# Kernel optimization log

Measured on AMD Instinct MI355X. Metric: run time of the kernel, lower is better.

The kernel has to match this reference:

```python
import jax, jax.numpy as jnp
import numpy as np

N_PTS = 65536      # query points (ray samples)
N_NODES = 4096     # deformation-graph nodes
K = 20             # neighbors, hardcoded in the module
D_PE = 32          # positional-encoding channels (sliced off, unused)
DIS_THRESH = 0.00021
FAR_VAL = 1e9


def setup_inputs() -> dict:
    key = jax.random.key(0)
    k1, k2, k3, k4, k5 = jax.random.split(key, 5)
    inputs = jax.random.normal(k1, (N_PTS, 3 + D_PE), dtype=jnp.float32)
    vd = jax.random.normal(k2, (N_NODES, 3), dtype=jnp.float32)
    R = jax.random.normal(k3, (N_NODES, 3, 3), dtype=jnp.float32)
    g = jax.random.normal(k4, (N_NODES, 3), dtype=jnp.float32)
    t = jax.random.normal(k5, (N_NODES, 3), dtype=jnp.float32) * 0.1
    return {"inputs": inputs, "vd": vd, "R": R, "g": g, "t": t}


def reference(inputs, vd, R, g, t):
    pts = inputs[:, :3]  # [N,3]; inputs[:,3:] (positional encoding) is unused

    # --- KNN (knn_points semantics: squared L2 dists, ascending) ---
    d2 = (jnp.sum(pts * pts, axis=-1, keepdims=True)
          + jnp.sum(vd * vd, axis=-1)[None, :]
          - 2.0 * pts @ vd.T)                      # [N, n]
    neg_d, idx = jax.lax.top_k(-d2, K)             # smallest d2 first
    dis = -neg_d                                   # [N,K] squared dists, ascending

    # --- neighbor weights: w = (1 - d/d_max)^2, normalized ---
    dis_max = jnp.max(dis, axis=-1, keepdims=True)
    w = jnp.square(1.0 - dis / dis_max)
    w = w / jnp.sum(w, axis=-1, keepdims=True)     # [N,K] (K=20 > 1, so no ones override)

    # --- per-neighbor gather + rigid transform: p = R^T (x - g - t) + g ---
    Rg = R[idx]                                    # [N,K,3,3]
    gg = g[idx]                                    # [N,K,3]
    tg = t[idx]                                    # [N,K,3]
    x = pts[:, None, :] - gg - tg                  # [N,K,3]
    p = jnp.einsum('nkji,nkj->nki', Rg, x) + gg    # R^T @ x, [N,K,3]
    R_inv = jnp.swapaxes(Rg, -1, -2)               # [N,K,3,3]

    # --- weighted blend over K neighbors ---
    p_blend = jnp.sum(p * w[:, :, None], axis=1)               # [N,3]
    R_blend = jnp.sum(R_inv * w[:, :, None, None], axis=1)     # [N,3,3]

    # --- far-point masking on x-coordinate ---
    far = dis[:, 0] > DIS_THRESH
    p_blend = p_blend.at[:, 0].set(jnp.where(far, FAR_VAL, p_blend[:, 0]))
    return p_blend, R_blend
```

## Files before the change

### kernel.cpp

```cpp
#include <hip/hip_runtime.h>
#include <stdint.h>


#define NPTS   65536
#define NNODES 4096
#define KSEL   20
#define CAP    32
#define BT     256
#define AFRAG_BYTES  (NNODES * 64)
#define WS_NEEDED    AFRAG_BYTES

typedef __attribute__((ext_vector_type(8)))  short short8;
typedef __attribute__((ext_vector_type(16))) float f32x16;

__device__ __forceinline__ uint32_t umin32(uint32_t a, uint32_t b) { return a < b ? a : b; }
__device__ __forceinline__ uint32_t umax32(uint32_t a, uint32_t b) { return a > b ? a : b; }
__device__ __forceinline__ void cmpswap(uint32_t& a, uint32_t& b) {
  const uint32_t lo = umin32(a, b), hi = umax32(a, b); a = lo; b = hi;
}
__device__ __forceinline__ void insert20(uint32_t m[KSEL], uint32_t x) {
#pragma unroll
  for (int k = KSEL - 1; k >= 1; --k)
    m[k] = umin32(m[k], umax32(m[k - 1], x));
  m[0] = umin32(m[0], x);
}
__device__ __forceinline__ float thr_from(uint32_t m19) {
  return __uint_as_float(umin32((m19 >> 12) << 11, 0x7F7FFFFFu));
}
__device__ __forceinline__ unsigned short f2bf(float x) {
  uint32_t u = __float_as_uint(x);
  return (unsigned short)((u + 0x7FFFu + ((u >> 16) & 1u)) >> 16);
}
__device__ __forceinline__ float bf2f(unsigned short h) {
  return __uint_as_float(((uint32_t)h) << 16);
}

__global__ void dg_prep(const float* __restrict__ vd,
                        unsigned short* __restrict__ aF) {
  const int j = blockIdx.x * 256 + threadIdx.x;
  const float v0 = vd[j * 3 + 0], v1 = vd[j * 3 + 1], v2 = vd[j * 3 + 2];
  unsigned short H[3], M[3], L[3];
  const float vc[3] = {v0, v1, v2};
#pragma unroll
  for (int c = 0; c < 3; ++c) {
    H[c] = f2bf(vc[c]);
    const float r1 = vc[c] - bf2f(H[c]);
    M[c] = f2bf(r1);
    const float r2 = r1 - bf2f(M[c]);
    L[c] = f2bf(r2);
  }
  const float sv = v0 * v0 + v1 * v1 + v2 * v2;
  const unsigned short svH = f2bf(sv);
  const float rs1 = sv - bf2f(svH);
  const unsigned short svM = f2bf(rs1);
  const unsigned short svL = f2bf(rs1 - bf2f(svM));

  unsigned short* o = aF + j * 32;
  o[0]=H[0]; o[1]=H[1]; o[2]=H[2]; o[3]=M[0]; o[4]=M[1]; o[5]=M[2];
  o[6]=L[0]; o[7]=L[1]; o[8]=L[2]; o[9]=H[0]; o[10]=H[1]; o[11]=H[2];
  o[12]=M[0]; o[13]=M[1]; o[14]=M[2]; o[15]=L[0];
  o[16]=L[1]; o[17]=L[2]; o[18]=H[0]; o[19]=H[1]; o[20]=H[2];
  o[21]=M[0]; o[22]=M[1]; o[23]=M[2];
  o[24]=L[0]; o[25]=L[1]; o[26]=L[2];
  o[27]=(unsigned short)svH; o[28]=(unsigned short)svM; o[29]=(unsigned short)svL;
  o[30]=0x3F80; o[31]=0x3F80;
}

__global__ __launch_bounds__(BT, 4) void dg_mfma(
    const float* __restrict__ inp, const float* __restrict__ vd,
    const float* __restrict__ Rm, const float* __restrict__ gv,
    const float* __restrict__ tv, const short8* __restrict__ aF,
    float* __restrict__ out)
{
  __shared__ uint32_t st[CAP * BT];
  const int tid  = threadIdx.x;
  const int lane = tid & 63;
  const int col  = lane & 31;
  const int h    = lane >> 5;
  const int wv   = tid >> 6;
  const int half = wv & 1;
  const int pg   = wv >> 1;
  const int P    = pg * 32 + col;
  const int gi   = blockIdx.x * 64 + P;

  const float p0 = inp[gi * 35 + 0];
  const float p1 = inp[gi * 35 + 1];
  const float p2 = inp[gi * 35 + 2];
  const float sp = p0 * p0 + p1 * p1 + p2 * p2;

  unsigned short qH[3], qM[3], qL[3], spH, spM;
  {
    const float qc[3] = {-2.0f * p0, -2.0f * p1, -2.0f * p2};
#pragma unroll
    for (int c = 0; c < 3; ++c) {
      qH[c] = f2bf(qc[c]);
      const float r1 = qc[c] - bf2f(qH[c]);
      qM[c] = f2bf(r1);
      const float r2 = r1 - bf2f(qM[c]);
      qL[c] = f2bf(r2);
    }
    spH = f2bf(sp);
    spM = f2bf(sp - bf2f(spH));
  }
  short8 b1, b2;
  if (h == 0) {
    b1[0]=qH[0]; b1[1]=qH[1]; b1[2]=qH[2]; b1[3]=qH[0];
    b1[4]=qH[1]; b1[5]=qH[2]; b1[6]=qH[0]; b1[7]=qH[1];
    b2[0]=qM[1]; b2[1]=qM[2]; b2[2]=qL[0]; b2[3]=qL[1];
    b2[4]=qL[2]; b2[5]=qL[0]; b2[6]=qL[1]; b2[7]=qL[2];
  } else {
    b1[0]=qH[2]; b1[1]=qM[0]; b1[2]=qM[1]; b1[3]=qM[2];
    b1[4]=qM[0]; b1[5]=qM[1]; b1[6]=qM[2]; b1[7]=qM[0];
    b2[0]=qL[0]; b2[1]=qL[1]; b2[2]=qL[2];
    b2[3]=(short)0x3F80; b2[4]=(short)0x3F80; b2[5]=(short)0x3F80;
    b2[6]=(short)spH; b2[7]=(short)spM;
  }

  uint32_t m[KSEL];
#pragma unroll
  for (int k = 0; k < KSEL; ++k) m[k] = 0xFFFFFFFFu;
  uint32_t cnt = 0;
  float thr = __uint_as_float(0x7F7FFFFFu);

  auto drain = [&]() {
    for (uint32_t u = 0; u < cnt; ++u) {
      const uint32_t x = st[u * BT + tid];
      if (x < m[KSEL - 1]) insert20(m, x);
    }
    cnt = 0;
    uint32_t k19 = m[KSEL - 1];
    k19 = umin32(k19, (uint32_t)__shfl_xor((int)k19, 32));
    thr = thr_from(k19);
  };

  f32x16 zacc;
#pragma unroll
  for (int i = 0; i < 16; ++i) zacc[i] = 0.0f;

  uint32_t nb = 0;
  auto process = [&](const f32x16& acc) {
#pragma unroll
    for (int i = 0; i < 16; ++i) {
      const float d = acc[i];
      const uint32_t key =
          ((__float_as_uint(fmaxf(d, 0.0f)) & 0xFFFFF800u) << 1)
          + (nb + (uint32_t)((i & 3) + 8 * (i >> 2)));
      st[cnt * BT + tid] = key;
      cnt += (uint32_t)(d < thr);
    }
    if (__any((int)(cnt >= CAP - 16))) drain();
    nb += 32;
  };

  const int T0 = half * 64;
  const short8* ap = aF + ((T0 * 32 + col) * 4 + h);
  nb = (uint32_t)(T0 * 32 + 4 * h);

  short8 a1A = ap[0], a2A = ap[2]; ap += 128;
  f32x16 accA = __builtin_amdgcn_mfma_f32_32x32x16_bf16(a1A, b1, zacc, 0, 0, 0);
  accA = __builtin_amdgcn_mfma_f32_32x32x16_bf16(a2A, b2, accA, 0, 0, 0);
  short8 a1B = ap[0], a2B = ap[2]; ap += 128;
  f32x16 accB;

#pragma unroll 1
  for (int k = 0; k < 31; ++k) {
    accB = __builtin_amdgcn_mfma_f32_32x32x16_bf16(a1B, b1, zacc, 0, 0, 0);
    accB = __builtin_amdgcn_mfma_f32_32x32x16_bf16(a2B, b2, accB, 0, 0, 0);
    a1A = ap[0]; a2A = ap[2]; ap += 128;
    process(accA);
    accA = __builtin_amdgcn_mfma_f32_32x32x16_bf16(a1A, b1, zacc, 0, 0, 0);
    accA = __builtin_amdgcn_mfma_f32_32x32x16_bf16(a2A, b2, accA, 0, 0, 0);
    a1B = ap[0]; a2B = ap[2]; ap += 128;
    process(accB);
  }
  accB = __builtin_amdgcn_mfma_f32_32x32x16_bf16(a1B, b1, zacc, 0, 0, 0);
  accB = __builtin_amdgcn_mfma_f32_32x32x16_bf16(a2B, b2, accB, 0, 0, 0);
  process(accA);
  process(accB);
  drain();

  uint32_t arr[32];
#pragma unroll
  for (int k = 0; k < KSEL; ++k) arr[k] = m[k];
#pragma unroll
  for (int k = KSEL; k < 32; ++k) arr[k] = 0xFFFFFFFFu;
#pragma unroll
  for (int k = 0; k < 16; ++k) {
    const uint32_t sa = (uint32_t)__shfl_xor((int)arr[k],      32);
    const uint32_t sb = (uint32_t)__shfl_xor((int)arr[31 - k], 32);
    arr[k]      = umin32(arr[k],      sb);
    arr[31 - k] = umin32(arr[31 - k], sa);
  }
#pragma unroll
  for (int dd = 16; dd >= 1; dd >>= 1)
#pragma unroll
    for (int k = 0; k < 32; ++k)
      if ((k & dd) == 0) cmpswap(arr[k], arr[k | dd]);

  __syncthreads();
  if (half == 1 && h == 0) {
    uint32_t* mb = st + P * KSEL;
#pragma unroll
    for (int k = 0; k < KSEL; ++k) mb[k] = arr[k];
  }
  __syncthreads();
  if (half == 1) return;

  uint32_t sset[KSEL];
  {
    const uint32_t* mb = st + P * KSEL;
#pragma unroll
    for (int k = 0; k < KSEL; ++k)
      sset[k] = umin32(arr[k], mb[KSEL - 1 - k]);
  }

  int   id10[10];
  float d10[10];
  float dmn = 1e30f, dmx = -1e30f;
#pragma unroll
  for (int s = 0; s < 10; ++s) {
    const int idk = (int)(sset[2 * s + h] & 0xFFFu);
    id10[s] = idk;
    const float v0 = vd[idk * 3 + 0];
    const float v1 = vd[idk * 3 + 1];
    const float v2 = vd[idk * 3 + 2];
    const float sv2 = v0 * v0 + v1 * v1 + v2 * v2;
    const float dt  = p0 * v0 + p1 * v1 + p2 * v2;
    const float ddx = (sp + sv2) - 2.0f * dt;
    d10[s] = ddx;
    dmn = fminf(dmn, ddx);
    dmx = fmaxf(dmx, ddx);
  }
  dmx = fmaxf(dmx, __shfl_xor(dmx, 32));
  dmn = fminf(dmn, __shfl_xor(dmn, 32));

  const float invmax = 1.0f / dmx;
  float wsum = 0.0f, pb0 = 0.0f, pb1 = 0.0f, pb2 = 0.0f;
  float rb[9];
#pragma unroll
  for (int a2i = 0; a2i < 9; ++a2i) rb[a2i] = 0.0f;

#pragma unroll
  for (int s = 0; s < 10; ++s) {
    const int idk = id10[s];
    const float u = 1.0f - d10[s] * invmax;
    const float w = u * u;
    wsum += w;
    const float* Rp = Rm + idk * 9;
    const float r00 = Rp[0], r01 = Rp[1], r02 = Rp[2];
    const float r10 = Rp[3], r11 = Rp[4], r12 = Rp[5];
    const float r20 = Rp[6], r21 = Rp[7], r22 = Rp[8];
    const float g0 = gv[idk * 3 + 0];
    const float g1 = gv[idk * 3 + 1];
    const float g2 = gv[idk * 3 + 2];
    const float t0 = tv[idk * 3 + 0];
    const float t1 = tv[idk * 3 + 1];
    const float t2 = tv[idk * 3 + 2];
    const float x0 = p0 - g0 - t0;
    const float x1 = p1 - g1 - t1;
    const float x2 = p2 - g2 - t2;
    pb0 += w * (r00 * x0 + r10 * x1 + r20 * x2 + g0);
    pb1 += w * (r01 * x0 + r11 * x1 + r21 * x2 + g1);
    pb2 += w * (r02 * x0 + r12 * x1 + r22 * x2 + g2);
    rb[0] += w * r00; rb[1] += w * r10; rb[2] += w * r20;
    rb[3] += w * r01; rb[4] += w * r11; rb[5] += w * r21;
    rb[6] += w * r02; rb[7] += w * r12; rb[8] += w * r22;
  }

  wsum += __shfl_xor(wsum, 32);
  pb0  += __shfl_xor(pb0, 32);
  pb1  += __shfl_xor(pb1, 32);
  pb2  += __shfl_xor(pb2, 32);
#pragma unroll
  for (int a2i = 0; a2i < 9; ++a2i) rb[a2i] += __shfl_xor(rb[a2i], 32);

  if (h == 0) {
    const float inw = 1.0f / wsum;
    float o0 = pb0 * inw;
    if (dmn > 0.00021f) o0 = 1000000000.0f;
    float* po = out + (size_t)gi * 3;
    po[0] = o0; po[1] = pb1 * inw; po[2] = pb2 * inw;
    float* ro = out + (size_t)NPTS * 3 + (size_t)gi * 9;
#pragma unroll
    for (int a2i = 0; a2i < 9; ++a2i) ro[a2i] = rb[a2i] * inw;
  }
}

__global__ __launch_bounds__(BT, 4) void dg_fb(
    const float* __restrict__ inp, const float* __restrict__ vd,
    const float* __restrict__ Rm, const float* __restrict__ gv,
    const float* __restrict__ tv, float* __restrict__ out)
{
  __shared__ uint32_t st[33 * BT];
  const int tid = threadIdx.x;
  const int q   = (tid >> 4) & 3;
  const int pl  = tid & 15;
  const int wv  = tid >> 6;
  const int gi  = blockIdx.x * 64 + wv * 16 + pl;
  const float p0 = inp[gi * 35 + 0];
  const float p1 = inp[gi * 35 + 1];
  const float p2 = inp[gi * 35 + 2];
  const float sp = p0 * p0 + p1 * p1 + p2 * p2;
  uint32_t m[KSEL];
#pragma unroll
  for (int k = 0; k < KSEL; ++k) m[k] = 0xFFFFFFFFu;
  int cnt = 0;
  float thr = __uint_as_float(0x7F7FFFFFu);
  const int jbase = q * (NNODES / 4);
  int lo = 0;
#pragma unroll
  for (int c = 0; c < 6; ++c) {
    const int hi = 32 << c;
    for (int i = lo; i < hi; ++i) {
      const int j = jbase + i;
      const float v0 = vd[j * 3 + 0], v1 = vd[j * 3 + 1], v2 = vd[j * 3 + 2];
      const float sv = v0 * v0 + v1 * v1 + v2 * v2;
      const float dt = p0 * v0 + p1 * v1 + p2 * v2;
      float d2 = fmaxf((sp + sv) - 2.0f * dt, 0.0f);
      if (d2 < thr) {
        st[cnt * BT + tid] = ((__float_as_uint(d2) & 0xFFFFF800u) << 1) | (uint32_t)j;
        if (++cnt == 33) {
          for (int u = 0; u < cnt; ++u) {
            const uint32_t x = st[u * BT + tid];
            if (x < m[KSEL - 1]) insert20(m, x);
          }
          cnt = 0; thr = thr_from(m[KSEL - 1]);
        }
      }
    }
    for (int u = 0; u < cnt; ++u) {
      const uint32_t x = st[u * BT + tid];
      if (x < m[KSEL - 1]) insert20(m, x);
    }
    cnt = 0; thr = thr_from(m[KSEL - 1]); lo = hi;
  }
  uint32_t arr[32];
#pragma unroll
  for (int k = 0; k < KSEL; ++k) arr[k] = m[k];
#pragma unroll
  for (int k = KSEL; k < 32; ++k) arr[k] = 0xFFFFFFFFu;
#pragma unroll
  for (int mask = 32; mask >= 16; mask >>= 1) {
#pragma unroll
    for (int k = 0; k < 16; ++k) {
      const uint32_t sa = (uint32_t)__shfl_xor((int)arr[k],      mask);
      const uint32_t sb = (uint32_t)__shfl_xor((int)arr[31 - k], mask);
      arr[k]      = umin32(arr[k],      sb);
      arr[31 - k] = umin32(arr[31 - k], sa);
    }
#pragma unroll
    for (int dd = 16; dd >= 1; dd >>= 1)
#pragma unroll
      for (int k = 0; k < 32; ++k)
        if ((k & dd) == 0) cmpswap(arr[k], arr[k | dd]);
  }
  int id5[5]; float d5[5];
  float dmn = 1e30f, dmx = -1e30f;
#pragma unroll
  for (int s = 0; s < 5; ++s) {
    const int idk = (int)(arr[4 * s + q] & 0xFFFu);
    id5[s] = idk;
    const float v0 = vd[idk * 3 + 0], v1 = vd[idk * 3 + 1], v2 = vd[idk * 3 + 2];
    const float sv = v0 * v0 + v1 * v1 + v2 * v2;
    const float dt = p0 * v0 + p1 * v1 + p2 * v2;
    const float ddx = (sp + sv) - 2.0f * dt;
    d5[s] = ddx; dmn = fminf(dmn, ddx); dmx = fmaxf(dmx, ddx);
  }
#pragma unroll
  for (int r = 16; r <= 32; r <<= 1) {
    dmx = fmaxf(dmx, __shfl_xor(dmx, r));
    dmn = fminf(dmn, __shfl_xor(dmn, r));
  }
  const float invmax = 1.0f / dmx;
  float wsum = 0.0f, pb0 = 0.0f, pb1 = 0.0f, pb2 = 0.0f;
  float rb[9];
#pragma unroll
  for (int a2i = 0; a2i < 9; ++a2i) rb[a2i] = 0.0f;
#pragma unroll
  for (int s = 0; s < 5; ++s) {
    const int idk = id5[s];
    const float u = 1.0f - d5[s] * invmax;
    const float w = u * u;
    wsum += w;
    const float* Rp = Rm + idk * 9;
    const float r00 = Rp[0], r01 = Rp[1], r02 = Rp[2];
    const float r10 = Rp[3], r11 = Rp[4], r12 = Rp[5];
    const float r20 = Rp[6], r21 = Rp[7], r22 = Rp[8];
    const float g0 = gv[idk * 3 + 0], g1 = gv[idk * 3 + 1], g2 = gv[idk * 3 + 2];
    const float t0 = tv[idk * 3 + 0], t1 = tv[idk * 3 + 1], t2 = tv[idk * 3 + 2];
    const float x0 = p0 - g0 - t0, x1 = p1 - g1 - t1, x2 = p2 - g2 - t2;
    pb0 += w * (r00 * x0 + r10 * x1 + r20 * x2 + g0);
    pb1 += w * (r01 * x0 + r11 * x1 + r21 * x2 + g1);
    pb2 += w * (r02 * x0 + r12 * x1 + r22 * x2 + g2);
    rb[0] += w * r00; rb[1] += w * r10; rb[2] += w * r20;
    rb[3] += w * r01; rb[4] += w * r11; rb[5] += w * r21;
    rb[6] += w * r02; rb[7] += w * r12; rb[8] += w * r22;
  }
#pragma unroll
  for (int r = 16; r <= 32; r <<= 1) {
    wsum += __shfl_xor(wsum, r);
    pb0 += __shfl_xor(pb0, r);
    pb1 += __shfl_xor(pb1, r);
    pb2 += __shfl_xor(pb2, r);
#pragma unroll
    for (int a2i = 0; a2i < 9; ++a2i) rb[a2i] += __shfl_xor(rb[a2i], r);
  }
  if (q == 0) {
    const float inw = 1.0f / wsum;
    float o0 = pb0 * inw;
    if (dmn > 0.00021f) o0 = 1000000000.0f;
    float* po = out + (size_t)gi * 3;
    po[0] = o0; po[1] = pb1 * inw; po[2] = pb2 * inw;
    float* ro = out + (size_t)NPTS * 3 + (size_t)gi * 9;
#pragma unroll
    for (int a2i = 0; a2i < 9; ++a2i) ro[a2i] = rb[a2i] * inw;
  }
}

extern "C" void kernel_launch(void* const* d_in, const int* in_sizes, int n_in,
                              void* d_out, int out_size, void* d_ws, size_t ws_size,
                              hipStream_t stream) {
  const float* inp = (const float*)d_in[0];
  const float* vd  = (const float*)d_in[1];
  const float* Rm  = (const float*)d_in[2];
  const float* gv  = (const float*)d_in[3];
  const float* tv  = (const float*)d_in[4];
  float* out = (float*)d_out;

  if (ws_size >= (size_t)WS_NEEDED) {
    unsigned short* aF = (unsigned short*)d_ws;
    dg_prep<<<NNODES / 256, 256, 0, stream>>>(vd, aF);
    dg_mfma<<<NPTS / 64, BT, 0, stream>>>(inp, vd, Rm, gv, tv,
                                          (const short8*)aF, out);
  } else {
    dg_fb<<<NPTS / 64, BT, 0, stream>>>(inp, vd, Rm, gv, tv, out);
  }
}
```

Before: 153.4 us.

## Halve MFMA block to 32 points and replace serial drain with bitonic merge

The MFMA KNN kernel now uses 128-thread blocks, each handling 32 points with two waves splitting the node range, and launches twice as many blocks. The candidate drain loop changes from a data-dependent serial insertion into the top-20 list to a fixed bitonic sort of the 32-entry buffer, merged with the current list and sorted again. This removes divergent variable-length loops in favour of branch-free compare-swap networks, at the cost of more fixed ALU work and register pressure per drain (launch bounds relaxed to allow it). The fallback kernel is pinned to its old 256-thread configuration.

```diff
diff --git a/kernel.cpp b/kernel.cpp
--- a/kernel.cpp
+++ b/kernel.cpp
@@ -6,7 +6,7 @@
 #define NNODES 4096
 #define KSEL   20
 #define CAP    32
-#define BT     256
+#define BT     128
 #define AFRAG_BYTES  (NNODES * 64)
 #define WS_NEEDED    AFRAG_BYTES
 
@@ -17,6 +17,13 @@
 __device__ __forceinline__ uint32_t umax32(uint32_t a, uint32_t b) { return a > b ? a : b; }
 __device__ __forceinline__ void cmpswap(uint32_t& a, uint32_t& b) {
   const uint32_t lo = umin32(a, b), hi = umax32(a, b); a = lo; b = hi;
+}
+__device__ __forceinline__ void sort32(uint32_t arr[32]) {
+#pragma unroll
+  for (int dd = 16; dd >= 1; dd >>= 1)
+#pragma unroll
+    for (int k = 0; k < 32; ++k)
+      if ((k & dd) == 0) cmpswap(arr[k], arr[k | dd]);
 }
 __device__ __forceinline__ void insert20(uint32_t m[KSEL], uint32_t x) {
 #pragma unroll
@@ -66,7 +73,7 @@
   o[30]=0x3F80; o[31]=0x3F80;
 }
 
-__global__ __launch_bounds__(BT, 4) void dg_mfma(
+__global__ __launch_bounds__(BT, 2) void dg_mfma(
     const float* __restrict__ inp, const float* __restrict__ vd,
     const float* __restrict__ Rm, const float* __restrict__ gv,
     const float* __restrict__ tv, const short8* __restrict__ aF,
@@ -77,11 +84,8 @@
   const int lane = tid & 63;
   const int col  = lane & 31;
   const int h    = lane >> 5;
-  const int wv   = tid >> 6;
-  const int half = wv & 1;
-  const int pg   = wv >> 1;
-  const int P    = pg * 32 + col;
-  const int gi   = blockIdx.x * 64 + P;
+  const int half = tid >> 6;
+  const int gi   = blockIdx.x * 32 + col;
 
   const float p0 = inp[gi * 35 + 0];
   const float p1 = inp[gi * 35 + 1];
@@ -123,10 +127,25 @@
   float thr = __uint_as_float(0x7F7FFFFFu);
 
   auto drain = [&]() {
-    for (uint32_t u = 0; u < cnt; ++u) {
+    uint32_t c[32];
+#pragma unroll
+    for (int u = 0; u < 32; ++u) {
       const uint32_t x = st[u * BT + tid];
-      if (x < m[KSEL - 1]) insert20(m, x);
-    }
+      c[u] = ((uint32_t)u < cnt) ? x : 0xFFFFFFFFu;
+    }
+    sort32(c);
+#pragma unroll
+    for (int k = 0; k < 16; ++k) {
+      const uint32_t mk  = (k < KSEL)        ? m[k]      : 0xFFFFFFFFu;
+      const uint32_t mk2 = ((31 - k) < KSEL) ? m[31 - k] : 0xFFFFFFFFu;
+      const uint32_t t1 = umin32(mk,  c[31 - k]);
+      const uint32_t t2 = umin32(mk2, c[k]);
+      c[k]      = t1;
+      c[31 - k] = t2;
+    }
+    sort32(c);
+#pragma unroll
+    for (int k = 0; k < KSEL; ++k) m[k] = c[k];
     cnt = 0;
     uint32_t k19 = m[KSEL - 1];
     k19 = umin32(k19, (uint32_t)__shfl_xor((int)k19, 32));
@@ -191,15 +210,11 @@
     arr[k]      = umin32(arr[k],      sb);
     arr[31 - k] = umin32(arr[31 - k], sa);
   }
-#pragma unroll
-  for (int dd = 16; dd >= 1; dd >>= 1)
-#pragma unroll
-    for (int k = 0; k < 32; ++k)
-      if ((k & dd) == 0) cmpswap(arr[k], arr[k | dd]);
+  sort32(arr);
 
   __syncthreads();
   if (half == 1 && h == 0) {
-    uint32_t* mb = st + P * KSEL;
+    uint32_t* mb = st + col * KSEL;
 #pragma unroll
     for (int k = 0; k < KSEL; ++k) mb[k] = arr[k];
   }
@@ -208,7 +223,7 @@
 
   uint32_t sset[KSEL];
   {
-    const uint32_t* mb = st + P * KSEL;
+    const uint32_t* mb = st + col * KSEL;
 #pragma unroll
     for (int k = 0; k < KSEL; ++k)
       sset[k] = umin32(arr[k], mb[KSEL - 1 - k]);
@@ -286,12 +301,12 @@
   }
 }
 
-__global__ __launch_bounds__(BT, 4) void dg_fb(
+__global__ __launch_bounds__(256, 4) void dg_fb(
     const float* __restrict__ inp, const float* __restrict__ vd,
     const float* __restrict__ Rm, const float* __restrict__ gv,
     const float* __restrict__ tv, float* __restrict__ out)
 {
-  __shared__ uint32_t st[33 * BT];
+  __shared__ uint32_t st[33 * 256];
   const int tid = threadIdx.x;
   const int q   = (tid >> 4) & 3;
   const int pl  = tid & 15;
@@ -318,10 +333,10 @@
       const float dt = p0 * v0 + p1 * v1 + p2 * v2;
       float d2 = fmaxf((sp + sv) - 2.0f * dt, 0.0f);
       if (d2 < thr) {
-        st[cnt * BT + tid] = ((__float_as_uint(d2) & 0xFFFFF800u) << 1) | (uint32_t)j;
+        st[cnt * 256 + tid] = ((__float_as_uint(d2) & 0xFFFFF800u) << 1) | (uint32_t)j;
         if (++cnt == 33) {
           for (int u = 0; u < cnt; ++u) {
-            const uint32_t x = st[u * BT + tid];
+            const uint32_t x = st[u * 256 + tid];
             if (x < m[KSEL - 1]) insert20(m, x);
           }
           cnt = 0; thr = thr_from(m[KSEL - 1]);
@@ -329,7 +344,7 @@
       }
     }
     for (int u = 0; u < cnt; ++u) {
-      const uint32_t x = st[u * BT + tid];
+      const uint32_t x = st[u * 256 + tid];
       if (x < m[KSEL - 1]) insert20(m, x);
     }
     cnt = 0; thr = thr_from(m[KSEL - 1]); lo = hi;
@@ -430,9 +445,9 @@
   if (ws_size >= (size_t)WS_NEEDED) {
     unsigned short* aF = (unsigned short*)d_ws;
     dg_prep<<<NNODES / 256, 256, 0, stream>>>(vd, aF);
-    dg_mfma<<<NPTS / 64, BT, 0, stream>>>(inp, vd, Rm, gv, tv,
+    dg_mfma<<<NPTS / 32, BT, 0, stream>>>(inp, vd, Rm, gv, tv,
                                           (const short8*)aF, out);
   } else {
-    dg_fb<<<NPTS / 64, BT, 0, stream>>>(inp, vd, Rm, gv, tv, out);
-  }
-}
+    dg_fb<<<NPTS / 64, 256, 0, stream>>>(inp, vd, Rm, gv, tv, out);
+  }
+}
```

After: 137.1 us. 10.6% less time.
